# Optimization experiments

Hardware: AMD Instinct MI355X
Metric: run time of the kernel (lower is better)

Reference implementation:

```python
import jax, jax.numpy as jnp
import numpy as np

N, E, T, D, H = 30000, 200000, 400000, 128, 8
F = D // H            # out_feat = 16
CLASS_NUM = 6
PI = 3.1415926        # constant used in original code


def layer_norm(x, g, b, eps=1e-5):
    m = x.mean(-1, keepdims=True)
    v = ((x - m) ** 2).mean(-1, keepdims=True)
    return (x - m) * jax.lax.rsqrt(v + eps) * g + b


def setup_inputs() -> dict:
    key = jax.random.key(0)
    ks = jax.random.split(key, 20)
    s = 1.0 / np.sqrt(D)
    s2 = 1.0 / np.sqrt(2 * D)
    inp = {
        "bond_embedding": jax.random.normal(ks[0], (E, D), jnp.float32) * 0.1,
        "pos": jax.random.normal(ks[1], (N, 3), jnp.float32),
        "basic_attn": jax.random.uniform(ks[2], (E, 1), jnp.float32),
        "ang_table": jax.random.normal(ks[3], (CLASS_NUM, D), jnp.float32) * 0.1,
        "ang_in_W": jax.random.normal(ks[4], (D, D), jnp.float32) * s,
        "ang_in_b": jnp.zeros((D,), jnp.float32),
        "ang2_W": jax.random.normal(ks[5], (D, D), jnp.float32) * s,
        "ang2_b": jnp.zeros((D,), jnp.float32),
        "ang1_W": jax.random.normal(ks[6], (D, D), jnp.float32) * s,
        "ang1_b": jnp.zeros((D,), jnp.float32),
        "k_W": jax.random.normal(ks[7], (D, D), jnp.float32) * s,
        "q_W": jax.random.normal(ks[8], (D, D), jnp.float32) * s,
        "v_W": jax.random.normal(ks[9], (D, D), jnp.float32) * s,
        "dis_W": jax.random.normal(ks[10], (1, H), jnp.float32) * 0.1,
        "ffn_W1": jax.random.normal(ks[11], (D, 2 * D), jnp.float32) * s,
        "ffn_W2": jax.random.normal(ks[12], (2 * D, D), jnp.float32) * s2,
        "ln1_g": jnp.ones((D,), jnp.float32),
        "ln1_b": jnp.zeros((D,), jnp.float32),
        "ln2_g": jnp.ones((D,), jnp.float32),
        "ln2_b": jnp.zeros((D,), jnp.float32),
        "index_kj": jax.random.randint(ks[13], (T,), 0, E, jnp.int32),
        "index_ji": jax.random.randint(ks[14], (T,), 0, E, jnp.int32),
        "idx_i": jax.random.randint(ks[15], (T,), 0, N, jnp.int32),
        "idx_j": jax.random.randint(ks[16], (T,), 0, N, jnp.int32),
        "idx_k": jax.random.randint(ks[17], (T,), 0, N, jnp.int32),
    }
    return inp


def reference(bond_embedding, pos, basic_attn, ang_table, ang_in_W, ang_in_b,
              ang2_W, ang2_b, ang1_W, ang1_b, k_W, q_W, v_W, dis_W,
              ffn_W1, ffn_W2, ln1_g, ln1_b, ln2_g, ln2_b,
              index_kj, index_ji, idx_i, idx_j, idx_k):
    # --- triplet geometry -> angle ---
    pos_i = pos[idx_i]
    pos_ji = pos[idx_j] - pos_i                       # [T, 3]
    pos_ki = pos[idx_k] - pos_i                       # [T, 3]
    a = (pos_ji * pos_ki).sum(-1)                     # dot
    b = jnp.linalg.norm(jnp.cross(pos_ji, pos_ki), axis=-1)
    angle = jnp.arctan2(b, a)                         # [T], in [0, pi]

    # --- angle embedding (discretize, embed, 3 dense+ReLU layers) ---
    bins = jnp.clip((angle / (PI / CLASS_NUM)).astype(jnp.int32), 0, CLASS_NUM - 1)
    ae = ang_table[bins]                              # [T, D]
    ae = jax.nn.relu(ae @ ang_in_W + ang_in_b)        # angle_input_layer
    ae = jax.nn.relu(ae @ ang2_W + ang2_b)            # angle2
    ae = jax.nn.relu(ae @ ang1_W + ang1_b)            # angle1
    ae = ae.reshape(-1, H, F)                         # [T, H, F]

    # --- distance decay per triplet, per head ---
    dd = (basic_attn[index_kj] @ dis_W)[:, :, None]   # [T, H, 1]

    # --- k/q/v projections, triplet gather ---
    k = (bond_embedding @ k_W).reshape(-1, H, F)
    q = (bond_embedding @ q_W).reshape(-1, H, F)
    v = (bond_embedding @ v_W).reshape(-1, H, F)
    feat_kj = k[index_kj] + ae                        # [T, H, F]
    feat_ji = q[index_ji] + ae
    feat_v = v[index_kj] + ae

    # --- unnormalized attention, exp, scatter-add softmax over index_ji ---
    att = (feat_kj * feat_ji).sum(-1, keepdims=True) / jnp.sqrt(jnp.float32(F))
    att = jnp.exp(att + dd)                           # [T, H, 1]
    denom = jax.ops.segment_sum(att, index_ji, num_segments=E)  # [E, H, 1]
    att = att / denom[index_ji]

    # --- weighted scatter-add aggregation ---
    v_att = (feat_v * att).reshape(-1, D)             # [T, D]
    msg = jax.ops.segment_sum(v_att, index_ji, num_segments=E)  # [E, D]
    he = msg + bond_embedding                         # beta=False path

    # --- FFN with pre-LN and post-LN residual ---
    h = layer_norm(he, ln1_g, ln1_b)
    h = jax.nn.relu(h @ ffn_W1) @ ffn_W2
    return layer_norm(h + he, ln2_g, ln2_b)
```

## Files before the change

### kernel.cpp

```cpp
#include <hip/hip_runtime.h>
#include <cstdint>
#include <math.h>

#define N_ATOMS 30000
#define E_EDGES 200000
#define T_TRI   400000
#define D_DIM   128
#define H_HEADS 8
#define F_FEAT  16
#define CLS     6

typedef __attribute__((ext_vector_type(8))) short bf16x8;
typedef __attribute__((ext_vector_type(4))) float f32x4;

static __device__ __forceinline__ unsigned short f2bf(float f) {
    union { float f; unsigned u; } v; v.f = f;
    unsigned r = v.u + 0x7FFFu + ((v.u >> 16) & 1u);
    return (unsigned short)(r >> 16);
}
static __device__ __forceinline__ void bf2x(unsigned u, float& a, float& b) {
    union { unsigned u; float f; } x, y;
    x.u = u << 16; y.u = u & 0xFFFF0000u;
    a = x.f; b = y.f;
}
static __device__ __forceinline__ float bf2f(unsigned short u) {
    union { unsigned u; float f; } x; x.u = ((unsigned)u) << 16; return x.f;
}

__launch_bounds__(256)
__global__ void ang_mlp_kernel(const float* __restrict__ tab,
                               const float* __restrict__ W0, const float* __restrict__ b0,
                               const float* __restrict__ W1, const float* __restrict__ b1,
                               const float* __restrict__ W2, const float* __restrict__ b2,
                               float* __restrict__ out)
{
    __shared__ float bufA[CLS * D_DIM];
    __shared__ float bufB[CLS * D_DIM];
    __shared__ float Wl[D_DIM * D_DIM];
    const int tid = threadIdx.x;
    for (int i = tid; i < CLS * D_DIM; i += 256) bufA[i] = tab[i];
    const float* Ws[3] = {W0, W1, W2};
    const float* bs[3] = {b0, b1, b2};
    float* in  = bufA;
    float* ob  = bufB;
    for (int l = 0; l < 3; ++l) {
        __syncthreads();
        for (int i = tid * 4; i < D_DIM * D_DIM; i += 256 * 4)
            *(float4*)&Wl[i] = *(const float4*)&Ws[l][i];
        __syncthreads();
        for (int o = tid; o < CLS * D_DIM; o += 256) {
            const int r = o >> 7, c = o & 127;
            float acc = bs[l][c];
            #pragma unroll 8
            for (int k = 0; k < D_DIM; ++k) acc += in[r * D_DIM + k] * Wl[k * D_DIM + c];
            ob[o] = fmaxf(acc, 0.f);
        }
        float* t = in; in = ob; ob = t;
    }
    __syncthreads();
    for (int i = tid; i < CLS * D_DIM; i += 256) out[i] = in[i];
}

__launch_bounds__(256)
__global__ void tri_bins_kernel(const float* __restrict__ pos,
                                const int* __restrict__ idx_i,
                                const int* __restrict__ idx_j,
                                const int* __restrict__ idx_k,
                                const int* __restrict__ iji,
                                int* __restrict__ bins,
                                int* __restrict__ cnt)
{
    const int t = blockIdx.x * 256 + threadIdx.x;
    if (t >= T_TRI) return;
    const int ii = idx_i[t], jj = idx_j[t], kk = idx_k[t];
    const float pix = pos[3*ii], piy = pos[3*ii+1], piz = pos[3*ii+2];
    const float jx = __fsub_rn(pos[3*jj],   pix);
    const float jy = __fsub_rn(pos[3*jj+1], piy);
    const float jz = __fsub_rn(pos[3*jj+2], piz);
    const float kx = __fsub_rn(pos[3*kk],   pix);
    const float ky = __fsub_rn(pos[3*kk+1], piy);
    const float kz = __fsub_rn(pos[3*kk+2], piz);
    const float a  = __fadd_rn(__fadd_rn(__fmul_rn(jx,kx), __fmul_rn(jy,ky)),
                               __fmul_rn(jz,kz));
    const float cx = __fsub_rn(__fmul_rn(jy,kz), __fmul_rn(jz,ky));
    const float cy = __fsub_rn(__fmul_rn(jz,kx), __fmul_rn(jx,kz));
    const float cz = __fsub_rn(__fmul_rn(jx,ky), __fmul_rn(jy,kx));
    const float ss = __fadd_rn(__fadd_rn(__fmul_rn(cx,cx), __fmul_rn(cy,cy)),
                               __fmul_rn(cz,cz));
    const float b  = __fsqrt_rn(ss);

    int bin;
    if (b == 0.0f && __float_as_uint(a) == 0x80000000u) {
        bin = 0;
    } else {
        const float angle = (float)atan2((double)b, (double)a);
        const float c = (float)(3.1415926 / 6.0);
        const float q = __fdiv_rn(angle, c);
        bin = (int)q;
        bin = bin < 0 ? 0 : (bin > CLS - 1 ? CLS - 1 : bin);
    }
    bins[t] = bin;
    atomicAdd(&cnt[iji[t]], 1);
}

__launch_bounds__(256)
__global__ void scan1_kernel(const int* __restrict__ cnt, int* __restrict__ offs,
                             int* __restrict__ bsum)
{
    __shared__ int buf[256];
    const int i = blockIdx.x * 256 + threadIdx.x;
    const int v = (i < E_EDGES) ? cnt[i] : 0;
    buf[threadIdx.x] = v;
    __syncthreads();
    for (int o = 1; o < 256; o <<= 1) {
        const int t = (threadIdx.x >= o) ? buf[threadIdx.x - o] : 0;
        __syncthreads();
        buf[threadIdx.x] += t;
        __syncthreads();
    }
    if (i < E_EDGES) offs[i] = buf[threadIdx.x] - v;
    if (threadIdx.x == 255) bsum[blockIdx.x] = buf[255];
}

__launch_bounds__(1024)
__global__ void scan2_kernel(int* __restrict__ bsum, int nb)
{
    __shared__ int buf[1024];
    const int tid = threadIdx.x;
    const int v = (tid < nb) ? bsum[tid] : 0;
    buf[tid] = v;
    __syncthreads();
    for (int o = 1; o < 1024; o <<= 1) {
        const int t = (tid >= o) ? buf[tid - o] : 0;
        __syncthreads();
        buf[tid] += t;
        __syncthreads();
    }
    if (tid < nb) bsum[tid] = buf[tid] - v;
}

__launch_bounds__(256)
__global__ void scan3_kernel(int* __restrict__ offs, const int* __restrict__ bsum)
{
    const int i = blockIdx.x * 256 + threadIdx.x;
    if (i < E_EDGES) offs[i] += bsum[blockIdx.x];
}

__launch_bounds__(256)
__global__ void fill_kernel(const int* __restrict__ iji, const int* __restrict__ offs,
                            int* __restrict__ cur, int* __restrict__ slot)
{
    const int t = blockIdx.x * 256 + threadIdx.x;
    if (t >= T_TRI) return;
    const int e = iji[t];
    const int p = offs[e] + atomicAdd(&cur[e], 1);
    slot[p] = t;
}

__launch_bounds__(256)
__global__ void conv_w_kernel(const float* __restrict__ kW, const float* __restrict__ qW,
                              const float* __restrict__ vW,
                              const float* __restrict__ W1, const float* __restrict__ W2,
                              unsigned short* __restrict__ Wt,
                              unsigned short* __restrict__ W1t,
                              unsigned short* __restrict__ W2t)
{
    const int i = blockIdx.x * 256 + threadIdx.x;
    if (i < 384 * 128) {
        const int n = i >> 7, k = i & 127;
        const int sel = n >> 7, c = n & 127;
        const float* W = (sel == 0) ? kW : (sel == 1) ? qW : vW;
        Wt[i] = f2bf(W[k * 128 + c]);
    }
    if (i < 128 * 256) {
        { const int n = i >> 7, k = i & 127;  W1t[n * 128 + k] = f2bf(W1[k * 256 + n]); }
        { const int n = i >> 8, k = i & 255;  W2t[n * 256 + k] = f2bf(W2[k * 128 + n]); }
    }
}

__launch_bounds__(256)
__global__ void proj_mfma(const float* __restrict__ bond,
                          const unsigned short* __restrict__ Wt,
                          unsigned short* __restrict__ KVh,
                          unsigned short* __restrict__ Qh)
{
    __shared__ unsigned short ms[64 * 392];
    const int lane = threadIdx.x & 63, w = threadIdx.x >> 6;
    const int base_row = blockIdx.x * 64;
    const int lr = lane & 15, g = lane >> 4;
    f32x4 acc[4][6];
    #pragma unroll
    for (int m = 0; m < 4; ++m)
        #pragma unroll
        for (int n = 0; n < 6; ++n) acc[m][n] = (f32x4){0.f, 0.f, 0.f, 0.f};
    #pragma unroll
    for (int kk = 0; kk < 4; ++kk) {
        bf16x8 a[4], b[6];
        #pragma unroll
        for (int m = 0; m < 4; ++m) {
            const int64_t ab = (int64_t)(base_row + m * 16 + lr) * 128 + kk * 32 + g * 8;
            const float4 f0 = *(const float4*)&bond[ab];
            const float4 f1 = *(const float4*)&bond[ab + 4];
            a[m][0] = (short)f2bf(f0.x); a[m][1] = (short)f2bf(f0.y);
            a[m][2] = (short)f2bf(f0.z); a[m][3] = (short)f2bf(f0.w);
            a[m][4] = (short)f2bf(f1.x); a[m][5] = (short)f2bf(f1.y);
            a[m][6] = (short)f2bf(f1.z); a[m][7] = (short)f2bf(f1.w);
        }
        #pragma unroll
        for (int n = 0; n < 6; ++n)
            b[n] = *(const bf16x8*)&Wt[((w * 6 + n) * 16 + lr) * 128 + kk * 32 + g * 8];
        #pragma unroll
        for (int m = 0; m < 4; ++m)
            #pragma unroll
            for (int n = 0; n < 6; ++n)
                acc[m][n] = __builtin_amdgcn_mfma_f32_16x16x32_bf16(a[m], b[n], acc[m][n], 0, 0, 0);
    }
    #pragma unroll
    for (int m = 0; m < 4; ++m)
        #pragma unroll
        for (int n = 0; n < 6; ++n)
            #pragma unroll
            for (int r = 0; r < 4; ++r)
                ms[(m * 16 + g * 4 + r) * 392 + (w * 6 + n) * 16 + lr] = f2bf(acc[m][n][r]);
    __syncthreads();
    for (int idx = threadIdx.x; idx < 64 * 48; idx += 256) {
        const int row = idx / 48, c8 = (idx % 48) * 8;
        const int e = base_row + row;
        const uint4 v = *(const uint4*)&ms[row * 392 + c8];
        if (c8 < 128)       *(uint4*)&KVh[(int64_t)e * 256 + c8] = v;
        else if (c8 < 256)  *(uint4*)&Qh[(int64_t)e * 128 + (c8 - 128)] = v;
        else                *(uint4*)&KVh[(int64_t)e * 256 + 128 + (c8 - 256)] = v;
    }
}

__launch_bounds__(256)
__global__ void edge_att_kernel(const unsigned short* __restrict__ KVh,
                                const unsigned short* __restrict__ Qh,
                                const float* __restrict__ aeT,
                                const int* __restrict__ bins,
                                const int* __restrict__ ikj,
                                const int* __restrict__ slot,
                                const int* __restrict__ offs,
                                const int* __restrict__ cnt,
                                const float* __restrict__ battn,
                                const float* __restrict__ disW,
                                const float* __restrict__ bond,
                                const float* __restrict__ g1,
                                const float* __restrict__ b1,
                                unsigned short* __restrict__ hef,
                                unsigned short* __restrict__ hbf)
{
    __shared__ float aeL[CLS * D_DIM];
    for (int i = threadIdx.x; i < CLS * D_DIM; i += 256) aeL[i] = aeT[i];
    __syncthreads();
    const int wid  = threadIdx.x >> 6;
    const int lane = threadIdx.x & 63;
    const int e = blockIdx.x * 4 + wid;
    const int d0 = lane * 2;
    const int h  = lane >> 3;
    const float dw = disW[h];

    unsigned qw = *(const unsigned*)&Qh[(int64_t)e * D_DIM + d0];
    float q0, q1; bf2x(qw, q0, q1);

    float acc0 = 0.f, acc1 = 0.f, den = 0.f;
    const int start = offs[e], n = cnt[e];
    int bin = 0; unsigned kw = 0, vw = 0; float bat = 0.f;
    if (n > 0) {
        const int t0 = slot[start];
        bin = bins[t0];
        const int ekj0 = ikj[t0];
        const int64_t kvb = (int64_t)ekj0 * 256;
        kw = *(const unsigned*)&KVh[kvb + d0];
        vw = *(const unsigned*)&KVh[kvb + 128 + d0];
        bat = battn[ekj0];
    }
    for (int s = 0; s < n; ++s) {
        const int bin_c = bin;
        const unsigned kw_c = kw, vw_c = vw;
        const float bat_c = bat;
        if (s + 1 < n) {
            const int t1 = slot[start + s + 1];
            bin = bins[t1];
            const int ekj1 = ikj[t1];
            const int64_t kvb = (int64_t)ekj1 * 256;
            kw = *(const unsigned*)&KVh[kvb + d0];
            vw = *(const unsigned*)&KVh[kvb + 128 + d0];
            bat = battn[ekj1];
        }
        const float ae0 = aeL[bin_c * D_DIM + d0];
        const float ae1 = aeL[bin_c * D_DIM + d0 + 1];
        float k0, k1; bf2x(kw_c, k0, k1);
        float pd = (k0 + ae0) * (q0 + ae0) + (k1 + ae1) * (q1 + ae1);
        pd += __shfl_xor(pd, 1);
        pd += __shfl_xor(pd, 2);
        pd += __shfl_xor(pd, 4);
        const float ex = expf(pd * 0.25f + bat_c * dw);
        den += ex;
        float v0, v1; bf2x(vw_c, v0, v1);
        acc0 += ex * (v0 + ae0);
        acc1 += ex * (v1 + ae1);
    }
    const float inv = (den > 0.f) ? 1.f / den : 0.f;
    const int64_t base = (int64_t)e * D_DIM;
    const float x0 = acc0 * inv + bond[base + d0];
    const float x1 = acc1 * inv + bond[base + d0 + 1];
    *(unsigned*)&hef[base + d0] =
        (unsigned)f2bf(x0) | ((unsigned)f2bf(x1) << 16);
    float sum = x0 + x1;
    #pragma unroll
    for (int o = 32; o > 0; o >>= 1) sum += __shfl_xor(sum, o);
    const float mean = sum * (1.f / 128.f);
    const float dx0 = x0 - mean, dx1 = x1 - mean;
    float var = dx0 * dx0 + dx1 * dx1;
    #pragma unroll
    for (int o = 32; o > 0; o >>= 1) var += __shfl_xor(var, o);
    const float rs = rsqrtf(var * (1.f / 128.f) + 1e-5f);
    const float h0v = dx0 * rs * g1[d0]     + b1[d0];
    const float h1v = dx1 * rs * g1[d0 + 1] + b1[d0 + 1];
    *(unsigned*)&hbf[base + d0] =
        (unsigned)f2bf(h0v) | ((unsigned)f2bf(h1v) << 16);
}

__launch_bounds__(256)
__global__ void ffn_fused(const unsigned short* __restrict__ hbf,
                          const unsigned short* __restrict__ W1t,
                          const unsigned short* __restrict__ W2t,
                          const unsigned short* __restrict__ hef,
                          const float* __restrict__ g2, const float* __restrict__ b2,
                          float* __restrict__ outp)
{
    __shared__ __align__(16) unsigned char lds[64 * 264 * 2];
    unsigned short* ms = (unsigned short*)lds;
    float (*cs)[132] = (float(*)[132])lds;
    const int lane = threadIdx.x & 63, w = threadIdx.x >> 6;
    const int base_row = blockIdx.x * 64;
    const int lr = lane & 15, g = lane >> 4;

    unsigned short heu0[16], heu1[16];
    #pragma unroll
    for (int i = 0; i < 16; ++i) {
        const int64_t rg = (int64_t)(base_row + w * 16 + i) * 128;
        heu0[i] = hef[rg + lane];
        heu1[i] = hef[rg + 64 + lane];
    }

    {
        f32x4 acc[4][4];
        #pragma unroll
        for (int m = 0; m < 4; ++m)
            #pragma unroll
            for (int n = 0; n < 4; ++n) acc[m][n] = (f32x4){0.f, 0.f, 0.f, 0.f};
        #pragma unroll
        for (int kk = 0; kk < 4; ++kk) {
            bf16x8 a[4], b[4];
            #pragma unroll
            for (int m = 0; m < 4; ++m)
                a[m] = *(const bf16x8*)&hbf[(int64_t)(base_row + m * 16 + lr) * 128 + kk * 32 + g * 8];
            #pragma unroll
            for (int n = 0; n < 4; ++n)
                b[n] = *(const bf16x8*)&W1t[((w * 4 + n) * 16 + lr) * 128 + kk * 32 + g * 8];
            #pragma unroll
            for (int m = 0; m < 4; ++m)
                #pragma unroll
                for (int n = 0; n < 4; ++n)
                    acc[m][n] = __builtin_amdgcn_mfma_f32_16x16x32_bf16(a[m], b[n], acc[m][n], 0, 0, 0);
        }
        #pragma unroll
        for (int m = 0; m < 4; ++m)
            #pragma unroll
            for (int n = 0; n < 4; ++n)
                #pragma unroll
                for (int r = 0; r < 4; ++r) {
                    float v = acc[m][n][r];
                    v = v > 0.f ? v : 0.f;
                    ms[(m * 16 + g * 4 + r) * 264 + (w * 4 + n) * 16 + lr] = f2bf(v);
                }
    }
    __syncthreads();

    f32x4 acc2[4][2];
    #pragma unroll
    for (int m = 0; m < 4; ++m)
        #pragma unroll
        for (int n = 0; n < 2; ++n) acc2[m][n] = (f32x4){0.f, 0.f, 0.f, 0.f};
    #pragma unroll
    for (int kk = 0; kk < 8; ++kk) {
        bf16x8 a[4], b[2];
        #pragma unroll
        for (int m = 0; m < 4; ++m)
            a[m] = *(const bf16x8*)&ms[(m * 16 + lr) * 264 + kk * 32 + g * 8];
        #pragma unroll
        for (int n = 0; n < 2; ++n)
            b[n] = *(const bf16x8*)&W2t[((w * 2 + n) * 16 + lr) * 256 + kk * 32 + g * 8];
        #pragma unroll
        for (int m = 0; m < 4; ++m)
            #pragma unroll
            for (int n = 0; n < 2; ++n)
                acc2[m][n] = __builtin_amdgcn_mfma_f32_16x16x32_bf16(a[m], b[n], acc2[m][n], 0, 0, 0);
    }
    __syncthreads();
    #pragma unroll
    for (int m = 0; m < 4; ++m)
        #pragma unroll
        for (int n = 0; n < 2; ++n)
            #pragma unroll
            for (int r = 0; r < 4; ++r)
                cs[m * 16 + g * 4 + r][w * 32 + n * 16 + lr] = acc2[m][n][r];
    __syncthreads();

    #pragma unroll 2
    for (int i = 0; i < 16; ++i) {
        const int row = w * 16 + i;
        const int64_t rg = (int64_t)(base_row + row) * 128;
        float x0 = cs[row][lane]      + bf2f(heu0[i]);
        float x1 = cs[row][64 + lane] + bf2f(heu1[i]);
        float s = x0 + x1;
        #pragma unroll
        for (int o = 32; o > 0; o >>= 1) s += __shfl_xor(s, o);
        const float mean = s * (1.f / 128.f);
        const float d0 = x0 - mean, d1 = x1 - mean;
        float v = d0 * d0 + d1 * d1;
        #pragma unroll
        for (int o = 32; o > 0; o >>= 1) v += __shfl_xor(v, o);
        const float rs = rsqrtf(v * (1.f / 128.f) + 1e-5f);
        outp[rg + lane]      = d0 * rs * g2[lane]      + b2[lane];
        outp[rg + 64 + lane] = d1 * rs * g2[lane + 64] + b2[lane + 64];
    }
}

extern "C" void kernel_launch(void* const* d_in, const int* in_sizes, int n_in,
                              void* d_out, int out_size, void* d_ws, size_t ws_size,
                              hipStream_t stream)
{
    const float* bond     = (const float*)d_in[0];
    const float* pos      = (const float*)d_in[1];
    const float* battn    = (const float*)d_in[2];
    const float* ang_tab  = (const float*)d_in[3];
    const float* ang_in_W = (const float*)d_in[4];
    const float* ang_in_b = (const float*)d_in[5];
    const float* ang2_W   = (const float*)d_in[6];
    const float* ang2_b   = (const float*)d_in[7];
    const float* ang1_W   = (const float*)d_in[8];
    const float* ang1_b   = (const float*)d_in[9];
    const float* k_W      = (const float*)d_in[10];
    const float* q_W      = (const float*)d_in[11];
    const float* v_W      = (const float*)d_in[12];
    const float* dis_W    = (const float*)d_in[13];
    const float* ffn_W1   = (const float*)d_in[14];
    const float* ffn_W2   = (const float*)d_in[15];
    const float* ln1_g    = (const float*)d_in[16];
    const float* ln1_b    = (const float*)d_in[17];
    const float* ln2_g    = (const float*)d_in[18];
    const float* ln2_b    = (const float*)d_in[19];
    const int*   index_kj = (const int*)d_in[20];
    const int*   index_ji = (const int*)d_in[21];
    const int*   idx_i    = (const int*)d_in[22];
    const int*   idx_j    = (const int*)d_in[23];
    const int*   idx_k    = (const int*)d_in[24];

    float* ws = (float*)d_ws;
    int*            bins  = (int*)(ws + 0);
    int*            slot  = (int*)(ws + 400000);
    int*            offs  = (int*)(ws + 800000);
    int*            cnt   = (int*)(ws + 1000000);
    int*            cur   = (int*)(ws + 1200000);
    int*            bsum  = (int*)(ws + 1400000);
    float*          aeT   = ws + 1401088;
    unsigned short* W1t   = (unsigned short*)(ws + 1401856);
    unsigned short* W2t   = (unsigned short*)(ws + 1418240);
    unsigned short* Wt    = (unsigned short*)(ws + 1434624);
    unsigned short* hef   = (unsigned short*)(ws + 1459200);
    unsigned short* hbf   = (unsigned short*)(ws + 14259200);
    unsigned short* Qh    = (unsigned short*)(ws + 27059200);

    unsigned short* KVh = (unsigned short*)d_out;
    float*          out = (float*)d_out;

    hipMemsetAsync(cnt, 0, (size_t)2 * E_EDGES * sizeof(int), stream);

    ang_mlp_kernel<<<1, 256, 0, stream>>>(ang_tab, ang_in_W, ang_in_b,
                                          ang2_W, ang2_b, ang1_W, ang1_b, aeT);
    conv_w_kernel<<<192, 256, 0, stream>>>(k_W, q_W, v_W, ffn_W1, ffn_W2, Wt, W1t, W2t);
    tri_bins_kernel<<<(T_TRI + 255) / 256, 256, 0, stream>>>(
        pos, idx_i, idx_j, idx_k, index_ji, bins, cnt);

    const int NB = (E_EDGES + 255) / 256;
    scan1_kernel<<<NB, 256, 0, stream>>>(cnt, offs, bsum);
    scan2_kernel<<<1, 1024, 0, stream>>>(bsum, NB);
    scan3_kernel<<<NB, 256, 0, stream>>>(offs, bsum);
    fill_kernel<<<(T_TRI + 255) / 256, 256, 0, stream>>>(index_ji, offs, cur, slot);

    proj_mfma<<<E_EDGES / 64, 256, 0, stream>>>(bond, Wt, KVh, Qh);

    edge_att_kernel<<<E_EDGES / 4, 256, 0, stream>>>(
        KVh, Qh, aeT, bins, index_kj, slot, offs, cnt,
        battn, dis_W, bond, ln1_g, ln1_b, hef, hbf);

    ffn_fused<<<E_EDGES / 64, 256, 0, stream>>>(hbf, W1t, W2t, hef, ln2_g, ln2_b, out);
}
```

Baseline: 531.8 us.

## Move residual add and first LayerNorm from attention kernel into FFN kernel

The attention kernel now writes only the normalized aggregated message in bf16. The residual add with bond_embedding and the pre-FFN LayerNorm move into the FFN kernel, which stages the normalized rows in LDS for the first MFMA GEMM. This drops one bf16 intermediate buffer write and read (hbf), and the residual is now kept in fp32 registers rather than rounded to bf16. The trade-offs are that the FFN kernel reads fp32 bond again, needs more LDS (which may lower occupancy), and gains an extra LayerNorm pass plus a barrier before the GEMM.

```diff
diff --git a/kernel.cpp b/kernel.cpp
--- a/kernel.cpp
+++ b/kernel.cpp
@@ -244,11 +244,7 @@
                                 const int* __restrict__ cnt,
                                 const float* __restrict__ battn,
                                 const float* __restrict__ disW,
-                                const float* __restrict__ bond,
-                                const float* __restrict__ g1,
-                                const float* __restrict__ b1,
-                                unsigned short* __restrict__ hef,
-                                unsigned short* __restrict__ hbf)
+                                unsigned short* __restrict__ attf)
 {
     __shared__ float aeL[CLS * D_DIM];
     for (int i = threadIdx.x; i < CLS * D_DIM; i += 256) aeL[i] = aeT[i];
@@ -303,47 +299,52 @@
     }
     const float inv = (den > 0.f) ? 1.f / den : 0.f;
     const int64_t base = (int64_t)e * D_DIM;
-    const float x0 = acc0 * inv + bond[base + d0];
-    const float x1 = acc1 * inv + bond[base + d0 + 1];
-    *(unsigned*)&hef[base + d0] =
-        (unsigned)f2bf(x0) | ((unsigned)f2bf(x1) << 16);
-    float sum = x0 + x1;
-    #pragma unroll
-    for (int o = 32; o > 0; o >>= 1) sum += __shfl_xor(sum, o);
-    const float mean = sum * (1.f / 128.f);
-    const float dx0 = x0 - mean, dx1 = x1 - mean;
-    float var = dx0 * dx0 + dx1 * dx1;
-    #pragma unroll
-    for (int o = 32; o > 0; o >>= 1) var += __shfl_xor(var, o);
-    const float rs = rsqrtf(var * (1.f / 128.f) + 1e-5f);
-    const float h0v = dx0 * rs * g1[d0]     + b1[d0];
-    const float h1v = dx1 * rs * g1[d0 + 1] + b1[d0 + 1];
-    *(unsigned*)&hbf[base + d0] =
-        (unsigned)f2bf(h0v) | ((unsigned)f2bf(h1v) << 16);
-}
-
-__launch_bounds__(256)
-__global__ void ffn_fused(const unsigned short* __restrict__ hbf,
+    *(unsigned*)&attf[base + d0] =
+        (unsigned)f2bf(acc0 * inv) | ((unsigned)f2bf(acc1 * inv) << 16);
+}
+
+__launch_bounds__(256)
+__global__ void ffn_fused(const unsigned short* __restrict__ attf,
+                          const float* __restrict__ bond,
                           const unsigned short* __restrict__ W1t,
                           const unsigned short* __restrict__ W2t,
-                          const unsigned short* __restrict__ hef,
+                          const float* __restrict__ g1, const float* __restrict__ b1,
                           const float* __restrict__ g2, const float* __restrict__ b2,
                           float* __restrict__ outp)
 {
-    __shared__ __align__(16) unsigned char lds[64 * 264 * 2];
-    unsigned short* ms = (unsigned short*)lds;
-    float (*cs)[132] = (float(*)[132])lds;
+    __shared__ __align__(16) unsigned char lds[51200];
+    unsigned short* hs = (unsigned short*)lds;
+    unsigned short* ms = (unsigned short*)(lds + 17408);
+    float (*cs)[132]   = (float(*)[132])lds;
     const int lane = threadIdx.x & 63, w = threadIdx.x >> 6;
     const int base_row = blockIdx.x * 64;
     const int lr = lane & 15, g = lane >> 4;
 
-    unsigned short heu0[16], heu1[16];
+    float hev0[16], hev1[16];
     #pragma unroll
     for (int i = 0; i < 16; ++i) {
         const int64_t rg = (int64_t)(base_row + w * 16 + i) * 128;
-        heu0[i] = hef[rg + lane];
-        heu1[i] = hef[rg + 64 + lane];
-    }
+        hev0[i] = bf2f(attf[rg + lane])      + bond[rg + lane];
+        hev1[i] = bf2f(attf[rg + 64 + lane]) + bond[rg + 64 + lane];
+    }
+    const float g1a = g1[lane], g1b = g1[lane + 64];
+    const float b1a = b1[lane], b1b = b1[lane + 64];
+    #pragma unroll 2
+    for (int i = 0; i < 16; ++i) {
+        const int row = w * 16 + i;
+        float s = hev0[i] + hev1[i];
+        #pragma unroll
+        for (int o = 32; o > 0; o >>= 1) s += __shfl_xor(s, o);
+        const float mean = s * (1.f / 128.f);
+        const float dx0 = hev0[i] - mean, dx1 = hev1[i] - mean;
+        float var = dx0 * dx0 + dx1 * dx1;
+        #pragma unroll
+        for (int o = 32; o > 0; o >>= 1) var += __shfl_xor(var, o);
+        const float rs = rsqrtf(var * (1.f / 128.f) + 1e-5f);
+        hs[row * 136 + lane]      = f2bf(dx0 * rs * g1a + b1a);
+        hs[row * 136 + 64 + lane] = f2bf(dx1 * rs * g1b + b1b);
+    }
+    __syncthreads();
 
     {
         f32x4 acc[4][4];
@@ -356,7 +357,7 @@
             bf16x8 a[4], b[4];
             #pragma unroll
             for (int m = 0; m < 4; ++m)
-                a[m] = *(const bf16x8*)&hbf[(int64_t)(base_row + m * 16 + lr) * 128 + kk * 32 + g * 8];
+                a[m] = *(const bf16x8*)&hs[(m * 16 + lr) * 136 + kk * 32 + g * 8];
             #pragma unroll
             for (int n = 0; n < 4; ++n)
                 b[n] = *(const bf16x8*)&W1t[((w * 4 + n) * 16 + lr) * 128 + kk * 32 + g * 8];
@@ -413,8 +414,8 @@
     for (int i = 0; i < 16; ++i) {
         const int row = w * 16 + i;
         const int64_t rg = (int64_t)(base_row + row) * 128;
-        float x0 = cs[row][lane]      + bf2f(heu0[i]);
-        float x1 = cs[row][64 + lane] + bf2f(heu1[i]);
+        float x0 = cs[row][lane]      + hev0[i];
+        float x1 = cs[row][64 + lane] + hev1[i];
         float s = x0 + x1;
         #pragma unroll
         for (int o = 32; o > 0; o >>= 1) s += __shfl_xor(s, o);
@@ -470,9 +471,8 @@
     unsigned short* W1t   = (unsigned short*)(ws + 1401856);
     unsigned short* W2t   = (unsigned short*)(ws + 1418240);
     unsigned short* Wt    = (unsigned short*)(ws + 1434624);
-    unsigned short* hef   = (unsigned short*)(ws + 1459200);
-    unsigned short* hbf   = (unsigned short*)(ws + 14259200);
-    unsigned short* Qh    = (unsigned short*)(ws + 27059200);
+    unsigned short* attf  = (unsigned short*)(ws + 1459200);
+    unsigned short* Qh    = (unsigned short*)(ws + 14259200);
 
     unsigned short* KVh = (unsigned short*)d_out;
     float*          out = (float*)d_out;
@@ -494,8 +494,8 @@
     proj_mfma<<<E_EDGES / 64, 256, 0, stream>>>(bond, Wt, KVh, Qh);
 
     edge_att_kernel<<<E_EDGES / 4, 256, 0, stream>>>(
-        KVh, Qh, aeT, bins, index_kj, slot, offs, cnt,
-        battn, dis_W, bond, ln1_g, ln1_b, hef, hbf);
-
-    ffn_fused<<<E_EDGES / 64, 256, 0, stream>>>(hbf, W1t, W2t, hef, ln2_g, ln2_b, out);
-}
+        KVh, Qh, aeT, bins, index_kj, slot, offs, cnt, battn, dis_W, attf);
+
+    ffn_fused<<<E_EDGES / 64, 256, 0, stream>>>(attf, bond, W1t, W2t,
+                                                ln1_g, ln1_b, ln2_g, ln2_b, out);
+}
```

New measurement: 525.5 us. About the same (-1.2%).
